# Optimization experiments

Hardware: AMD Instinct MI355X
Metric: run time of the kernel (lower is better)

Reference implementation:

```python
import jax, jax.numpy as jnp
import numpy as np

V = 50000   # input_size == output_size (one-hot vocab)
H = 256     # hidden_size
B = 512     # batch_size
L = 1       # num_layers

def setup_inputs() -> dict:
    key = jax.random.key(0)
    ks = jax.random.split(key, 9)
    s = 1.0 / np.sqrt(H)  # torch default uniform(-1/sqrt(H), 1/sqrt(H))
    inp = {
        "input": jax.random.randint(ks[0], (B,), 0, V, dtype=jnp.int64 if jax.config.jax_enable_x64 else jnp.int32),
        "target": jax.random.randint(ks[1], (B,), 0, V, dtype=jnp.int64 if jax.config.jax_enable_x64 else jnp.int32),
        "hidden": jax.random.normal(ks[2], (L, B, H), dtype=jnp.float32),
        "w_ih": jax.random.uniform(ks[3], (3 * H, V), jnp.float32, -s, s),
        "w_hh": jax.random.uniform(ks[4], (3 * H, H), jnp.float32, -s, s),
        "b_ih": jax.random.uniform(ks[5], (3 * H,), jnp.float32, -s, s),
        "b_hh": jax.random.uniform(ks[6], (3 * H,), jnp.float32, -s, s),
        "w_out": jax.random.uniform(ks[7], (V, H), jnp.float32, -s, s),
        "b_out": jax.random.uniform(ks[8], (V,), jnp.float32, -s, s),
    }
    return inp

def reference(input, target, hidden, w_ih, w_hh, b_ih, b_hh, w_out, b_out):
    # one-hot(input) @ w_ih.T is exactly a row-gather from w_ih.T  -> (B, 3H)
    h0 = hidden[0]                              # (B, H), num_layers == 1
    x_proj = w_ih.T[input] + b_ih               # (B, 3H)
    h_proj = h0 @ w_hh.T + b_hh                 # (B, 3H)
    xr, xz, xn = jnp.split(x_proj, 3, axis=-1)
    hr, hz, hn = jnp.split(h_proj, 3, axis=-1)
    r = jax.nn.sigmoid(xr + hr)                 # reset gate
    z = jax.nn.sigmoid(xz + hz)                 # update gate
    n = jnp.tanh(xn + r * hn)                   # candidate
    h1 = (1.0 - z) * n + z * h0                 # (B, H)
    logit = jnp.tanh(h1 @ w_out.T + b_out)      # (B, V)
    return logit, h1[None]                      # (B,V), (1,B,H)
```

## Files before the change

kernel.cpp:

```cpp
#include <hip/hip_runtime.h>
#include <hip/hip_bf16.h>

#define VOCAB 50000
#define HID   256
#define BATCH 512
#define GH    768

typedef __attribute__((ext_vector_type(8))) __bf16 bf16x8;
typedef __attribute__((ext_vector_type(4))) float f32x4;
typedef __attribute__((ext_vector_type(4))) unsigned int u32x4;

union BFrag {
    bf16x8 v;
    u32x4  q;
    __bf16 b[8];
};

__device__ __forceinline__ float fast_sigmoid(float x) {
    return 1.0f / (1.0f + __expf(-x));
}
__device__ __forceinline__ float fast_tanh(float x) {
    return 1.0f - 2.0f / (1.0f + __expf(2.0f * x));
}

__device__ __forceinline__ void cvt8(BFrag& t, f32x4 lo, f32x4 hi) {
    t.b[0] = (__bf16)lo.x; t.b[1] = (__bf16)lo.y;
    t.b[2] = (__bf16)lo.z; t.b[3] = (__bf16)lo.w;
    t.b[4] = (__bf16)hi.x; t.b[5] = (__bf16)hi.y;
    t.b[6] = (__bf16)hi.z; t.b[7] = (__bf16)hi.w;
}

template <int EPI, int ASRC, int NTB>
__global__ __launch_bounds__(256, 4) void gemm_db(
    const void* __restrict__ Asrc, const float* __restrict__ Bm,
    float* __restrict__ C, const float* __restrict__ bias,
    int Ncols, int mChunks)
{
    __shared__ char ldsA[2][32 * 512];

    const int tid  = threadIdx.x;
    const int wid  = tid >> 6;
    const int lane = tid & 63;
    const int r    = lane & 15;
    const int g    = lane >> 4;
    const int col  = blockIdx.x * 64 + wid * 16 + r;
    const int bcol = col < Ncols ? col : (Ncols - 1);

    BFrag bf[8];
    {
        const f32x4* wrow = reinterpret_cast<const f32x4*>(Bm + (size_t)bcol * 256);
        #pragma unroll
        for (int kk = 0; kk < 8; kk++) {
            f32x4 lo, hi;
            if (NTB) {
                lo = __builtin_nontemporal_load(&wrow[kk * 8 + g * 2]);
                hi = __builtin_nontemporal_load(&wrow[kk * 8 + g * 2 + 1]);
            } else {
                lo = wrow[kk * 8 + g * 2];
                hi = wrow[kk * 8 + g * 2 + 1];
            }
            cvt8(bf[kk], lo, hi);
        }
    }
    #pragma unroll
    for (int kk = 0; kk < 8; kk++)
        asm volatile("" : "+v"(bf[kk].q));
    float biasv = 0.0f;
    if (EPI == 1) biasv = bias[bcol];

    u32x4 areg[4];
    auto load_chunk = [&](int c) {
        const int mbase = (blockIdx.y * mChunks + c) * 32;
        if (ASRC == 1) {
            const u32x4* src = reinterpret_cast<const u32x4*>(
                (const unsigned short*)Asrc + (size_t)mbase * 256);
            #pragma unroll
            for (int i = 0; i < 4; i++) areg[i] = src[tid + i * 256];
        } else {
            const f32x4* src = reinterpret_cast<const f32x4*>(
                (const float*)Asrc + (size_t)mbase * 256);
            #pragma unroll
            for (int i = 0; i < 4; i++) {
                int u = tid + i * 256;
                BFrag t; cvt8(t, src[2 * u], src[2 * u + 1]);
                areg[i] = t.q;
            }
        }
    };
    auto write_lds = [&](int buf) {
        #pragma unroll
        for (int i = 0; i < 4; i++) {
            int u = tid + i * 256;
            int row = u >> 5, j = u & 31;
            int byte = row * 512 + ((j ^ (row & 7)) << 4);
            *reinterpret_cast<u32x4*>(&ldsA[buf][byte]) = areg[i];
        }
    };

    load_chunk(0);
    write_lds(0);
    if (mChunks > 1) load_chunk(1);
    asm volatile("s_waitcnt lgkmcnt(0)\n\ts_barrier" ::: "memory");

    for (int c = 0; c < mChunks; c++) {
        const int cur = c & 1;
        if (c + 1 < mChunks) {
            write_lds(cur ^ 1);
            if (c + 2 < mChunks) load_chunk(c + 2);
        }

        f32x4 acc[2];
        acc[0] = (f32x4){0.f, 0.f, 0.f, 0.f};
        acc[1] = (f32x4){0.f, 0.f, 0.f, 0.f};

        #pragma unroll
        for (int kk = 0; kk < 8; kk++) {
            #pragma unroll
            for (int m = 0; m < 2; m++) {
                int arow = m * 16 + r;
                int byte = arow * 512 + (((kk * 4 + g) ^ (arow & 7)) << 4);
                BFrag a;
                a.q = *reinterpret_cast<const u32x4*>(&ldsA[cur][byte]);
                acc[m] = __builtin_amdgcn_mfma_f32_16x16x32_bf16(a.v, bf[kk].v, acc[m], 0, 0, 0);
            }
        }

        if (col < Ncols) {
            const int rowbase = (blockIdx.y * mChunks + c) * 32 + g * 4;
            #pragma unroll
            for (int m = 0; m < 2; m++) {
                #pragma unroll
                for (int j = 0; j < 4; j++) {
                    float v = acc[m][j];
                    if (EPI == 1) v = fast_tanh(v + biasv);
                    C[(size_t)(rowbase + m * 16 + j) * Ncols + col] = v;
                }
            }
        }

        if (c + 1 < mChunks)
            asm volatile("s_waitcnt lgkmcnt(0)\n\ts_barrier" ::: "memory");
    }
}

__global__ __launch_bounds__(256) void gru_gate(
    const int* __restrict__ inp, const float* __restrict__ hidden,
    const float* __restrict__ w_ih, const float* __restrict__ b_ih,
    const float* __restrict__ b_hh, const float* __restrict__ hproj,
    float* __restrict__ h1out, unsigned short* __restrict__ h1bf)
{
    const int b = blockIdx.x;
    const int k = threadIdx.x;
    const int c = inp[b];

    float xr = w_ih[(size_t)k * VOCAB + c]         + b_ih[k];
    float xz = w_ih[(size_t)(k + 256) * VOCAB + c] + b_ih[k + 256];
    float xn = w_ih[(size_t)(k + 512) * VOCAB + c] + b_ih[k + 512];

    float hr = hproj[b * GH + k]       + b_hh[k];
    float hz = hproj[b * GH + 256 + k] + b_hh[k + 256];
    float hn = hproj[b * GH + 512 + k] + b_hh[k + 512];

    float rg = fast_sigmoid(xr + hr);
    float zg = fast_sigmoid(xz + hz);
    float ng = fast_tanh(xn + rg * hn);
    float h0 = hidden[b * HID + k];
    float h1 = (1.0f - zg) * ng + zg * h0;

    h1out[b * HID + k] = h1;
    __bf16 hb = (__bf16)h1;
    h1bf[b * HID + k] = __builtin_bit_cast(unsigned short, hb);
}

extern "C" void kernel_launch(void* const* d_in, const int* in_sizes, int n_in,
                              void* d_out, int out_size, void* d_ws, size_t ws_size,
                              hipStream_t stream) {
    const int*   input  = (const int*)  d_in[0];
    const float* hidden = (const float*)d_in[2];
    const float* w_ih   = (const float*)d_in[3];
    const float* w_hh   = (const float*)d_in[4];
    const float* b_ih   = (const float*)d_in[5];
    const float* b_hh   = (const float*)d_in[6];
    const float* w_out  = (const float*)d_in[7];
    const float* b_out  = (const float*)d_in[8];

    float* logit = (float*)d_out;
    float* h1    = (float*)d_out + (size_t)BATCH * VOCAB;

    float*          hproj = (float*)d_ws;
    unsigned short* h1bf  = (unsigned short*)((char*)d_ws + (size_t)BATCH * GH * 4);

    dim3 g1(GH / 64, BATCH / 32);
    gemm_db<0, 0, 0><<<g1, 256, 0, stream>>>(hidden, w_hh, hproj, nullptr, GH, 1);

    gru_gate<<<BATCH, 256, 0, stream>>>(input, hidden, w_ih, b_ih, b_hh, hproj,
                                        h1, h1bf);

    dim3 g3((VOCAB + 63) / 64, 1);
    gemm_db<1, 1, 1><<<g3, 256, 0, stream>>>(h1bf, w_out, logit, b_out, VOCAB, 16);
}
```

Baseline: 69.42 us.

## Switch GEMMs to 32x32x16 MFMA with 128-column tiles and split batch

Replaces the 16x16x32 bf16 MFMA tiling with 32x32x16, so each wave covers 32 columns and all 32 rows of a chunk, doubling the block's column tile to 128. The output GEMM now splits the batch over two blocks along y (8 chunks each), which adds parallelism but makes each w_out column tile get loaded and converted twice. Dimensions become template constants and the nontemporal loads on w_out are dropped. Register use grows from the 16 resident B fragments, which may reduce occupancy.

```diff
diff --git a/kernel.cpp b/kernel.cpp
--- a/kernel.cpp
+++ b/kernel.cpp
@@ -6,9 +6,10 @@
 #define BATCH 512
 #define GH    768
 
-typedef __attribute__((ext_vector_type(8))) __bf16 bf16x8;
-typedef __attribute__((ext_vector_type(4))) float f32x4;
-typedef __attribute__((ext_vector_type(4))) unsigned int u32x4;
+typedef __attribute__((ext_vector_type(8)))  __bf16 bf16x8;
+typedef __attribute__((ext_vector_type(4)))  float  f32x4;
+typedef __attribute__((ext_vector_type(16))) float  f32x16;
+typedef __attribute__((ext_vector_type(4)))  unsigned int u32x4;
 
 union BFrag {
     bf16x8 v;
@@ -30,47 +31,37 @@
     t.b[6] = (__bf16)hi.z; t.b[7] = (__bf16)hi.w;
 }
 
-template <int EPI, int ASRC, int NTB>
-__global__ __launch_bounds__(256, 4) void gemm_db(
+template <int EPI, int NCOLS, int MCHUNKS, int ASRC>
+__global__ __launch_bounds__(256, 4) void gemm32(
     const void* __restrict__ Asrc, const float* __restrict__ Bm,
-    float* __restrict__ C, const float* __restrict__ bias,
-    int Ncols, int mChunks)
+    float* __restrict__ C, const float* __restrict__ bias)
 {
     __shared__ char ldsA[2][32 * 512];
 
     const int tid  = threadIdx.x;
     const int wid  = tid >> 6;
     const int lane = tid & 63;
-    const int r    = lane & 15;
-    const int g    = lane >> 4;
-    const int col  = blockIdx.x * 64 + wid * 16 + r;
-    const int bcol = col < Ncols ? col : (Ncols - 1);
+    const int cw   = lane & 31;
+    const int h    = lane >> 5;
+    const int col  = blockIdx.x * 128 + wid * 32 + cw;
+    const int bcol = col < NCOLS ? col : (NCOLS - 1);
 
-    BFrag bf[8];
+    BFrag bf[16];
     {
         const f32x4* wrow = reinterpret_cast<const f32x4*>(Bm + (size_t)bcol * 256);
         #pragma unroll
-        for (int kk = 0; kk < 8; kk++) {
-            f32x4 lo, hi;
-            if (NTB) {
-                lo = __builtin_nontemporal_load(&wrow[kk * 8 + g * 2]);
-                hi = __builtin_nontemporal_load(&wrow[kk * 8 + g * 2 + 1]);
-            } else {
-                lo = wrow[kk * 8 + g * 2];
-                hi = wrow[kk * 8 + g * 2 + 1];
-            }
-            cvt8(bf[kk], lo, hi);
-        }
+        for (int ks = 0; ks < 16; ks++)
+            cvt8(bf[ks], wrow[ks * 4 + h * 2], wrow[ks * 4 + h * 2 + 1]);
     }
     #pragma unroll
-    for (int kk = 0; kk < 8; kk++)
-        asm volatile("" : "+v"(bf[kk].q));
+    for (int ks = 0; ks < 16; ks++)
+        asm volatile("" : "+v"(bf[ks].q));
     float biasv = 0.0f;
     if (EPI == 1) biasv = bias[bcol];
 
     u32x4 areg[4];
     auto load_chunk = [&](int c) {
-        const int mbase = (blockIdx.y * mChunks + c) * 32;
+        const int mbase = (blockIdx.y * MCHUNKS + c) * 32;
         if (ASRC == 1) {
             const u32x4* src = reinterpret_cast<const u32x4*>(
                 (const unsigned short*)Asrc + (size_t)mbase * 256);
@@ -99,46 +90,42 @@
 
     load_chunk(0);
     write_lds(0);
-    if (mChunks > 1) load_chunk(1);
+    if (MCHUNKS > 1) load_chunk(1);
     asm volatile("s_waitcnt lgkmcnt(0)\n\ts_barrier" ::: "memory");
 
-    for (int c = 0; c < mChunks; c++) {
+    for (int c = 0; c < MCHUNKS; c++) {
         const int cur = c & 1;
-        if (c + 1 < mChunks) {
+        if (c + 1 < MCHUNKS) {
             write_lds(cur ^ 1);
-            if (c + 2 < mChunks) load_chunk(c + 2);
+            if (c + 2 < MCHUNKS) load_chunk(c + 2);
         }
 
-        f32x4 acc[2];
-        acc[0] = (f32x4){0.f, 0.f, 0.f, 0.f};
-        acc[1] = (f32x4){0.f, 0.f, 0.f, 0.f};
+        f32x16 acc;
+        #pragma unroll
+        for (int i = 0; i < 16; i++) acc[i] = 0.0f;
 
         #pragma unroll
-        for (int kk = 0; kk < 8; kk++) {
-            #pragma unroll
-            for (int m = 0; m < 2; m++) {
-                int arow = m * 16 + r;
-                int byte = arow * 512 + (((kk * 4 + g) ^ (arow & 7)) << 4);
-                BFrag a;
-                a.q = *reinterpret_cast<const u32x4*>(&ldsA[cur][byte]);
-                acc[m] = __builtin_amdgcn_mfma_f32_16x16x32_bf16(a.v, bf[kk].v, acc[m], 0, 0, 0);
-            }
+        for (int ks = 0; ks < 16; ks++) {
+            int byte = cw * 512 + (((2 * ks + h) ^ (cw & 7)) << 4);
+            BFrag a;
+            a.q = *reinterpret_cast<const u32x4*>(&ldsA[cur][byte]);
+            acc = __builtin_amdgcn_mfma_f32_32x32x16_bf16(a.v, bf[ks].v, acc, 0, 0, 0);
         }
 
-        if (col < Ncols) {
-            const int rowbase = (blockIdx.y * mChunks + c) * 32 + g * 4;
+        if (col < NCOLS) {
+            const int rowb = (blockIdx.y * MCHUNKS + c) * 32 + h * 4;
             #pragma unroll
-            for (int m = 0; m < 2; m++) {
+            for (int q = 0; q < 4; q++) {
                 #pragma unroll
                 for (int j = 0; j < 4; j++) {
-                    float v = acc[m][j];
+                    float v = acc[q * 4 + j];
                     if (EPI == 1) v = fast_tanh(v + biasv);
-                    C[(size_t)(rowbase + m * 16 + j) * Ncols + col] = v;
+                    C[(size_t)(rowb + q * 8 + j) * NCOLS + col] = v;
                 }
             }
         }
 
-        if (c + 1 < mChunks)
+        if (c + 1 < MCHUNKS)
             asm volatile("s_waitcnt lgkmcnt(0)\n\ts_barrier" ::: "memory");
     }
 }
@@ -190,12 +177,12 @@
     float*          hproj = (float*)d_ws;
     unsigned short* h1bf  = (unsigned short*)((char*)d_ws + (size_t)BATCH * GH * 4);
 
-    dim3 g1(GH / 64, BATCH / 32);
-    gemm_db<0, 0, 0><<<g1, 256, 0, stream>>>(hidden, w_hh, hproj, nullptr, GH, 1);
+    dim3 g1(GH / 128, BATCH / 32);
+    gemm32<0, GH, 1, 0><<<g1, 256, 0, stream>>>(hidden, w_hh, hproj, nullptr);
 
     gru_gate<<<BATCH, 256, 0, stream>>>(input, hidden, w_ih, b_ih, b_hh, hproj,
                                         h1, h1bf);
 
-    dim3 g3((VOCAB + 63) / 64, 1);
-    gemm_db<1, 1, 1><<<g3, 256, 0, stream>>>(h1bf, w_out, logit, b_out, VOCAB, 16);
+    dim3 g3((VOCAB + 127) / 128, 2);
+    gemm32<1, VOCAB, 8, 1><<<g3, 256, 0, stream>>>(h1bf, w_out, logit, b_out);
 }
```

New measurement: 73.97 us. 6.6% more time.
